# Performance work log

Measured on AMD Instinct MI355X. Metric: run time of the kernel, lower is better.

Reference implementation:

```python
import jax, jax.numpy as jnp
import numpy as np
import math

IN_FEATURES = 512
KERNEL = 3
EPS = 1e-08
GAIN = 1.0 / math.sqrt(IN_FEATURES * KERNEL * KERNEL)  # lr_multiplier=1


def setup_inputs() -> dict:
    key = jax.random.key(0)
    k1, k2, k3 = jax.random.split(key, 3)
    x = jax.random.normal(k1, (16, 512, 32, 32), dtype=jnp.float32)
    style = jax.random.normal(k2, (16, 512), dtype=jnp.float32)
    weight = jax.random.normal(k3, (512, 512, 3, 3), dtype=jnp.float32)
    return {"x": x, "style": style, "weight": weight}


def reference(x, style, weight):
    # w: [B, O, I, k, k] = gain-scaled weight modulated per-sample by style over input channels
    w = (weight * GAIN)[None] * style[:, None, :, None, None]
    # demodulate: rsqrt of sum of squares over (I, kh, kw) per (B, O)
    sigma = jax.lax.rsqrt(jnp.sum(jnp.square(w), axis=(2, 3, 4)) + EPS)
    w = w * sigma[:, :, None, None, None]
    # per-sample conv2d with padding='same' (stride 1, k=3 -> pad 1)
    def conv_one(xi, wi):  # xi: [C,H,W], wi: [O,I,k,k]
        return jax.lax.conv_general_dilated(
            xi[None], wi, window_strides=(1, 1), padding='SAME',
            dimension_numbers=('NCHW', 'OIHW', 'NCHW'))[0]
    return jax.vmap(conv_one)(x, w)  # [B, O, H, W]
```

## Files before the change

### kernel.cpp

```cpp
#include <hip/hip_runtime.h>
#include <hip/hip_bf16.h>

#define EPSF 1e-8f
#define GAINF 0.014731391274719739f

typedef __attribute__((ext_vector_type(8))) __bf16 bf16x8;
typedef __attribute__((ext_vector_type(4))) __bf16 bf16x4;
typedef __attribute__((ext_vector_type(16))) float f32x16;

#define GLOAD_LDS16(gp, lp) __builtin_amdgcn_global_load_lds( \
    (const __attribute__((address_space(1))) unsigned int*)(gp), \
    (__attribute__((address_space(3))) unsigned int*)(lp), 16, 0, 0)

__global__ void k_prep(const float* __restrict__ x, const float* __restrict__ style,
                       const float* __restrict__ w, float* __restrict__ S,
                       __hip_bfloat16* __restrict__ wbf, __hip_bfloat16* __restrict__ xs) {
  int blk = blockIdx.x, tid = threadIdx.x;
  if (blk < 2048) {
    __shared__ float tile[64][65];
    int b = blk >> 7, rem = blk & 127, ct = rem >> 4, pt = rem & 15;
    int p0 = pt * 64, c0 = ct * 64;
    int tx = tid & 63, ty = tid >> 6;
#pragma unroll
    for (int k = 0; k < 16; ++k) {
      int ci = ty + k * 4;
      tile[ci][tx] = x[((b * 512) + (c0 + ci)) * 1024 + p0 + tx];
    }
    __syncthreads();
    int tq = tid & 15, py = tid >> 4;
    int c = c0 + tq * 4;
    int cb = c >> 5, cw = c & 31;
    float st0 = style[b * 512 + c], st1 = style[b * 512 + c + 1];
    float st2 = style[b * 512 + c + 2], st3 = style[b * 512 + c + 3];
#pragma unroll
    for (int k = 0; k < 4; ++k) {
      int pl = py + k * 16;
      int p = p0 + pl;
      int y = p >> 5, xx = p & 31;
      int site = (y + 1) * 34 + (xx + 1);
      bf16x4 v;
      v[0] = (__bf16)(tile[tq * 4 + 0][pl] * st0);
      v[1] = (__bf16)(tile[tq * 4 + 1][pl] * st1);
      v[2] = (__bf16)(tile[tq * 4 + 2][pl] * st2);
      v[3] = (__bf16)(tile[tq * 4 + 3][pl] * st3);
      *reinterpret_cast<bf16x4*>(xs + (size_t)(((b * 16 + cb) * 1156 + site) * 32 + cw)) = v;
    }
  } else if (blk < 3072) {
    int idx = (blk - 2048) * 256 + tid;
    int o = idx >> 9, i = idx & 511;
    const float* p = w + (size_t)idx * 9;
    float s = 0.f;
#pragma unroll
    for (int t = 0; t < 9; ++t) {
      float v = p[t];
      s += v * v;
      wbf[(size_t)t * 262144 + (i >> 5) * 16384 + o * 32 + (i & 31)] = __float2bfloat16(v);
    }
    S[idx] = s;
  } else {
    int bb = blk - 3072;
    int b = bb >> 4, cb = bb & 15;
    for (int i2 = tid; i2 < 528; i2 += 256) {
      int sb = i2 >> 2, q = i2 & 3;
      int yp, xp;
      if (sb < 34) { yp = 0; xp = sb; }
      else if (sb < 68) { yp = 33; xp = sb - 34; }
      else { int t2 = sb - 68; yp = 1 + (t2 >> 1); xp = (t2 & 1) * 33; }
      float4 z = {0.f, 0.f, 0.f, 0.f};
      *reinterpret_cast<float4*>(xs + (size_t)(((b * 16 + cb) * 1156 + yp * 34 + xp) * 32 + q * 8)) = z;
    }
  }
}

__global__ void k_sigma(const float* __restrict__ style, const float* __restrict__ S,
                        float* __restrict__ esc) {
  __shared__ float s2[8192];
  __shared__ float red[4][16];
  int tid = threadIdx.x, o = blockIdx.x;
  for (int idx = tid; idx < 8192; idx += 256) {
    float v = style[idx];
    s2[idx] = v * v;
  }
  __syncthreads();
  float acc[16];
#pragma unroll
  for (int b = 0; b < 16; ++b) acc[b] = 0.f;
  for (int i = tid; i < 512; i += 256) {
    float s = S[o * 512 + i];
#pragma unroll
    for (int b = 0; b < 16; ++b) acc[b] += s2[b * 512 + i] * s;
  }
#pragma unroll
  for (int b = 0; b < 16; ++b)
#pragma unroll
    for (int off = 32; off; off >>= 1) acc[b] += __shfl_down(acc[b], off);
  int lane = tid & 63, wv = tid >> 6;
  if (lane == 0)
#pragma unroll
    for (int b = 0; b < 16; ++b) red[wv][b] = acc[b];
  __syncthreads();
  if (tid < 16) {
    float s = red[0][tid] + red[1][tid] + red[2][tid] + red[3][tid];
    esc[tid * 512 + o] = GAINF * rsqrtf(s * (GAINF * GAINF) + EPSF);
  }
}

__global__ __launch_bounds__(256, 2) void k_conv(
    const __hip_bfloat16* __restrict__ wbf, const __hip_bfloat16* __restrict__ xs,
    const float* __restrict__ esc, float* __restrict__ out) {
  __shared__ __hip_bfloat16 ldsB[2 * 6528];
  int g = blockIdx.x;
  int xcd = g & 7, sblk = g >> 3;
  int mg = sblk >> 4;
  int n = xcd * 16 + (sblk & 15);
  int b = n >> 3, nt = n & 7;
  int row0 = nt * 4;
  int tid = threadIdx.x;
  int wv = tid >> 6, lane = tid & 63;
  int l31 = lane & 31, lhi = lane >> 5;
  int o_base = mg * 128 + wv * 32;

  int roff[4];
#pragma unroll
  for (int j = 0; j < 4; ++j) {
    int idx = wv * 204 + j * 64 + lane;
    int site = idx >> 2, q0 = idx & 3;
    int qs = q0 ^ ((site >> 1) & 3);
    roff[j] = site * 32 + qs * 8;
  }

#define STAGE(cbv) do { \
    const __hip_bfloat16* _g = xs + (size_t)((b * 16 + (cbv)) * 1156 + row0 * 34) * 32; \
    __hip_bfloat16* _l = ldsB + ((cbv) & 1) * 6528 + wv * 1632 + lane * 8; \
    _Pragma("unroll") \
    for (int _j = 0; _j < 3; ++_j) GLOAD_LDS16(_g + roff[_j], _l + _j * 512); \
    if (lane < 12) GLOAD_LDS16(_g + roff[3], _l + 3 * 512); \
  } while (0)

  int wrow = (o_base + l31) * 32 + lhi * 8;
#define LOADA(dst, t_, cb_) do { \
    const __hip_bfloat16* _p = wbf + (size_t)(t_) * 262144 + (cb_) * 16384 + wrow; \
    dst[0] = *reinterpret_cast<const bf16x8*>(_p); \
    dst[1] = *reinterpret_cast<const bf16x8*>(_p + 16); \
  } while (0)

  f32x16 acc[4];
#pragma unroll
  for (int j = 0; j < 4; ++j)
#pragma unroll
    for (int e = 0; e < 16; ++e) acc[j][e] = 0.f;

  bf16x8 aC[2], aN[2];
  STAGE(0);
  LOADA(aC, 0, 0);

  for (int cb = 0; cb < 16; ++cb) {
    __syncthreads();
    if (cb < 15) STAGE(cb + 1);
    const __hip_bfloat16* lb = ldsB + (cb & 1) * 6528;
#pragma unroll
    for (int t = 0; t < 9; ++t) {
      const int dy = t / 3, dx = t - dy * 3;
      if (cb < 15 || t < 8) {
        int tn = (t == 8) ? 0 : t + 1;
        int cbn = (t == 8) ? cb + 1 : cb;
        LOADA(aN, tn, cbn);
      }
      int s[4], sw[4];
#pragma unroll
      for (int ns = 0; ns < 4; ++ns) {
        s[ns] = (ns + dy) * 34 + l31 + dx;
        sw[ns] = (s[ns] >> 1) & 3;
      }
#pragma unroll
      for (int k2 = 0; k2 < 2; ++k2) {
        int ko = (k2 << 1) | lhi;
        bf16x8 bf[4];
#pragma unroll
        for (int ns = 0; ns < 4; ++ns)
          bf[ns] = *reinterpret_cast<const bf16x8*>(&lb[(s[ns] * 4 + (ko ^ sw[ns])) * 8]);
#pragma unroll
        for (int ns = 0; ns < 4; ++ns)
          acc[ns] = __builtin_amdgcn_mfma_f32_32x32x16_bf16(aC[k2], bf[ns], acc[ns], 0, 0, 0);
      }
      aC[0] = aN[0];
      aC[1] = aN[1];
    }
  }
  int pxb = nt * 128 + l31;
#pragma unroll
  for (int reg = 0; reg < 16; ++reg) {
    int o = o_base + (reg & 3) + ((reg >> 2) << 3) + (lhi << 2);
    float e = esc[(b << 9) + o];
#pragma unroll
    for (int ns = 0; ns < 4; ++ns)
      out[(size_t)((b << 9) + o) * 1024 + pxb + ns * 32] = acc[ns][reg] * e;
  }
#undef STAGE
#undef LOADA
}

extern "C" void kernel_launch(void* const* d_in, const int* in_sizes, int n_in,
                              void* d_out, int out_size, void* d_ws, size_t ws_size,
                              hipStream_t stream) {
  const float* x = (const float*)d_in[0];
  const float* style = (const float*)d_in[1];
  const float* w = (const float*)d_in[2];
  float* out = (float*)d_out;
  char* ws = (char*)d_ws;
  __hip_bfloat16* wbf = (__hip_bfloat16*)(ws);
  __hip_bfloat16* xs  = (__hip_bfloat16*)(ws + 4718592);
  float* S   = (float*)(ws + 23658496);
  float* esc = (float*)(ws + 24707072);

  hipLaunchKernelGGL(k_prep, dim3(3328), dim3(256), 0, stream, x, style, w, S, wbf, xs);
  hipLaunchKernelGGL(k_sigma, dim3(512), dim3(256), 0, stream, style, S, esc);
  hipLaunchKernelGGL(k_conv, dim3(512), dim3(256), 0, stream, wbf, xs, esc, out);
}
```

Baseline: 166.0 us.

## Reuse LDS B fragments across kernel rows and deepen A-fragment prefetch

```diff
diff --git a/kernel.cpp b/kernel.cpp
--- a/kernel.cpp
+++ b/kernel.cpp
@@ -150,41 +150,46 @@
 #pragma unroll
     for (int e = 0; e < 16; ++e) acc[j][e] = 0.f;
 
-  bf16x8 aC[2], aN[2];
+  bf16x8 aC[2], aN[2], aN2[2];
   STAGE(0);
   LOADA(aC, 0, 0);
+  LOADA(aN, 3, 0);
 
   for (int cb = 0; cb < 16; ++cb) {
     __syncthreads();
     if (cb < 15) STAGE(cb + 1);
     const __hip_bfloat16* lb = ldsB + (cb & 1) * 6528;
 #pragma unroll
-    for (int t = 0; t < 9; ++t) {
-      const int dy = t / 3, dx = t - dy * 3;
-      if (cb < 15 || t < 8) {
-        int tn = (t == 8) ? 0 : t + 1;
-        int cbn = (t == 8) ? cb + 1 : cb;
-        LOADA(aN, tn, cbn);
+    for (int dx = 0; dx < 3; ++dx) {
+      bf16x8 bw[2][6];
+#pragma unroll
+      for (int r = 0; r < 6; ++r) {
+        int s = r * 34 + l31 + dx;
+        int swz = (s >> 1) & 3;
+#pragma unroll
+        for (int k2 = 0; k2 < 2; ++k2) {
+          int ko = (k2 << 1) | lhi;
+          bw[k2][r] = *reinterpret_cast<const bf16x8*>(&lb[(s * 4 + (ko ^ swz)) * 8]);
+        }
       }
-      int s[4], sw[4];
-#pragma unroll
-      for (int ns = 0; ns < 4; ++ns) {
-        s[ns] = (ns + dy) * 34 + l31 + dx;
-        sw[ns] = (s[ns] >> 1) & 3;
+#pragma unroll
+      for (int dy = 0; dy < 3; ++dy) {
+        const int ti = dx * 3 + dy;
+        {
+          constexpr int tseq[11] = {0, 3, 6, 1, 4, 7, 2, 5, 8, 0, 3};
+          const int ti2 = ti + 2;
+          const int tn = tseq[ti2];
+          int cbn = (ti2 >= 9) ? cb + 1 : cb;
+          if (cbn < 16) LOADA(aN2, tn, cbn);
+        }
+#pragma unroll
+        for (int k2 = 0; k2 < 2; ++k2)
+#pragma unroll
+          for (int ns = 0; ns < 4; ++ns)
+            acc[ns] = __builtin_amdgcn_mfma_f32_32x32x16_bf16(aC[k2], bw[k2][dy + ns], acc[ns], 0, 0, 0);
+        aC[0] = aN[0]; aC[1] = aN[1];
+        aN[0] = aN2[0]; aN[1] = aN2[1];
       }
-#pragma unroll
-      for (int k2 = 0; k2 < 2; ++k2) {
-        int ko = (k2 << 1) | lhi;
-        bf16x8 bf[4];
-#pragma unroll
-        for (int ns = 0; ns < 4; ++ns)
-          bf[ns] = *reinterpret_cast<const bf16x8*>(&lb[(s[ns] * 4 + (ko ^ sw[ns])) * 8]);
-#pragma unroll
-        for (int ns = 0; ns < 4; ++ns)
-          acc[ns] = __builtin_amdgcn_mfma_f32_32x32x16_bf16(aC[k2], bf[ns], acc[ns], 0, 0, 0);
-      }
-      aC[0] = aN[0];
-      aC[1] = aN[1];
     }
   }
   int pxb = nt * 128 + l31;
```

New measurement: 174.8 us. +5.4%, slower.
